# Kernel tuning notes

Hardware: AMD Instinct MI355X
Metric: run time of the kernel (lower is better)

Reference implementation:

```python
import jax, jax.numpy as jnp
import numpy as np

NH = 8  # num_heads
EPS_LN = 1e-5
BN_DENOM = float(np.sqrt(1.0 + 1e-5))  # eval-mode BN with running_mean=0, running_var=1


def _layernorm(x, g, b):
    m = jnp.mean(x, axis=-1, keepdims=True)
    v = jnp.var(x, axis=-1, keepdims=True)
    return (x - m) * jax.lax.rsqrt(v + EPS_LN) * g + b


def _rope(q, k):
    # q,k: [B, H, T, D]
    t, d = q.shape[2], q.shape[3]
    half = d // 2
    pos = jnp.arange(t, dtype=q.dtype)[:, None]
    idx = jnp.arange(half, dtype=q.dtype)[None, :]
    inv_freq = 1.0 / (10000.0 ** (idx / half))
    ang = pos * inv_freq  # [T, half]
    sin = jnp.sin(ang)[None, None]
    cos = jnp.cos(ang)[None, None]

    def rot(x):
        x1, x2 = x[..., :half], x[..., half:]
        return jnp.concatenate([x1 * cos - x2 * sin, x1 * sin + x2 * cos], axis=-1)

    return rot(q), rot(k)


def _sep_conv(y, dw, pw):
    # y: [B, C, T]; dw: [C, 1, K]; pw: [O, C]
    c = y.shape[1]
    k = dw.shape[-1]
    y = jax.lax.conv_general_dilated(
        y, dw, window_strides=(2,), padding=[(k // 2, k // 2)],
        dimension_numbers=('NCH', 'OIH', 'NCH'), feature_group_count=c)
    return jnp.einsum('bct,oc->bot', y, pw)


def _attn(h, Wq, bq, Wk, bk, Wv, bv, Wo, bo):
    b, t, e = h.shape
    hd = e // NH
    scale = hd ** -0.5

    def split(z):
        return jnp.transpose(z.reshape(b, t, NH, hd), (0, 2, 1, 3))

    q = split(h @ Wq.T + bq)
    k = split(h @ Wk.T + bk)
    v = split(h @ Wv.T + bv)
    q, k = _rope(q, k)
    logits = jnp.einsum('bhtd,bhsd->bhts', q, k) * scale
    attn = jax.nn.softmax(logits, axis=-1)
    ctx = jnp.einsum('bhts,bhsd->bhtd', attn, v)
    ctx = jnp.transpose(ctx, (0, 2, 1, 3)).reshape(b, t, e)
    return ctx @ Wo.T + bo


def setup_inputs() -> dict:
    key = jax.random.key(0)
    ks = jax.random.split(key, 40)
    B, T, Cin = 8, 4096, 64
    E, L, MLP = 256, 6, 1024
    s = 0.02
    p = {}
    p['x'] = jax.random.normal(ks[0], (B, T, Cin), jnp.float32)
    p['conv1_dw'] = jax.random.normal(ks[1], (Cin, 1, 7), jnp.float32) * s
    p['conv1_pw'] = jax.random.normal(ks[2], (64, Cin), jnp.float32) * s
    p['bn1_g'] = jnp.ones((64,), jnp.float32)
    p['bn1_b'] = jnp.zeros((64,), jnp.float32)
    p['conv2_dw'] = jax.random.normal(ks[3], (64, 1, 7), jnp.float32) * s
    p['conv2_pw'] = jax.random.normal(ks[4], (128, 64), jnp.float32) * s
    p['bn2_g'] = jnp.ones((128,), jnp.float32)
    p['bn2_b'] = jnp.zeros((128,), jnp.float32)
    p['proj_w'] = jax.random.normal(ks[5], (E, 128), jnp.float32) * s
    p['proj_b'] = jnp.zeros((E,), jnp.float32)
    p['cls_tok'] = jax.random.normal(ks[6], (1, 1, E), jnp.float32) * s
    p['Wq'] = jax.random.normal(ks[7], (L, E, E), jnp.float32) * s
    p['bq'] = jnp.zeros((L, E), jnp.float32)
    p['Wk'] = jax.random.normal(ks[8], (L, E, E), jnp.float32) * s
    p['bk'] = jnp.zeros((L, E), jnp.float32)
    p['Wv'] = jax.random.normal(ks[9], (L, E, E), jnp.float32) * s
    p['bv'] = jnp.zeros((L, E), jnp.float32)
    p['Wo'] = jax.random.normal(ks[10], (L, E, E), jnp.float32) * s
    p['bo'] = jnp.zeros((L, E), jnp.float32)
    p['ln1_g'] = jnp.ones((L, E), jnp.float32)
    p['ln1_b'] = jnp.zeros((L, E), jnp.float32)
    p['mlp_w1'] = jax.random.normal(ks[11], (L, MLP, E), jnp.float32) * s
    p['mlp_b1'] = jnp.zeros((L, MLP), jnp.float32)
    p['mlp_w2'] = jax.random.normal(ks[12], (L, E, MLP), jnp.float32) * s
    p['mlp_b2'] = jnp.zeros((L, E), jnp.float32)
    p['ln2_g'] = jnp.ones((L, E), jnp.float32)
    p['ln2_b'] = jnp.zeros((L, E), jnp.float32)
    p['lat_w'] = jax.random.normal(ks[13], (E, E), jnp.float32) * s
    p['lat_b'] = jnp.zeros((E,), jnp.float32)
    p['latn_g'] = jnp.ones((E,), jnp.float32)
    p['latn_b'] = jnp.zeros((E,), jnp.float32)
    p['ts_w'] = jax.random.normal(ks[14], (1, E), jnp.float32) * s
    p['ts_b'] = jnp.zeros((1,), jnp.float32)
    return p


def reference(x, conv1_dw, conv1_pw, bn1_g, bn1_b, conv2_dw, conv2_pw, bn2_g, bn2_b,
              proj_w, proj_b, cls_tok, Wq, bq, Wk, bk, Wv, bv, Wo, bo,
              ln1_g, ln1_b, mlp_w1, mlp_b1, mlp_w2, mlp_b2, ln2_g, ln2_b,
              lat_w, lat_b, latn_g, latn_b, ts_w, ts_b):
    B = x.shape[0]
    y = jnp.transpose(x, (0, 2, 1))  # [B, C, T]
    y = _sep_conv(y, conv1_dw, conv1_pw)
    y = (y / BN_DENOM) * bn1_g[None, :, None] + bn1_b[None, :, None]
    y = jax.nn.gelu(y, approximate=False)
    y = _sep_conv(y, conv2_dw, conv2_pw)
    y = (y / BN_DENOM) * bn2_g[None, :, None] + bn2_b[None, :, None]
    y = jax.nn.gelu(y, approximate=False)
    y = jnp.transpose(y, (0, 2, 1))  # [B, T', 128]
    h = y @ proj_w.T + proj_b  # [B, T', E]
    h = jnp.concatenate([jnp.broadcast_to(cls_tok, (B, 1, h.shape[-1])), h], axis=1)
    L = Wq.shape[0]
    for i in range(L):
        a = _attn(h, Wq[i], bq[i], Wk[i], bk[i], Wv[i], bv[i], Wo[i], bo[i])
        h = _layernorm(h + a, ln1_g[i], ln1_b[i])
        m = jax.nn.gelu(h @ mlp_w1[i].T + mlp_b1[i], approximate=False) @ mlp_w2[i].T + mlp_b2[i]
        h = _layernorm(h + m, ln2_g[i], ln2_b[i])
    h = _layernorm(h @ lat_w.T + lat_b, latn_g, latn_b)
    logits = h[:, 1:] @ ts_w.T + ts_b  # per-time-step logits (CLS excluded)
    return logits
```

## Files before the change

### kernel.cpp

```cpp
#include <hip/hip_runtime.h>
#include <hip/hip_bf16.h>
#include <math.h>

typedef __hip_bfloat16 bf16;
typedef __attribute__((ext_vector_type(8))) short bf16x8_t;
typedef __attribute__((ext_vector_type(4))) short bf16x4_t;
typedef __attribute__((ext_vector_type(4))) float f32x4_t;

#define BN_RDENOM 0.9999950000374997f
#define EPS_LN 1e-5f
#define ATTN_SCALE 0.17677669529663687f
#define S_LEN 1025
#define S_PAD 1088
#define E_DIM 256
#define NHEAD 8
#define HDIM 32
#define MROWS (8 * S_LEN)
#define M_PAD 8320
#define WSLOT 786432

__device__ __forceinline__ float bf(const bf16 v) { return __bfloat162float(v); }
__device__ __forceinline__ bf16 tobf(float v) { return __float2bfloat16(v); }
__device__ __forceinline__ short bfbits(float v) {
    bf16 t = __float2bfloat16(v); short s; __builtin_memcpy(&s, &t, 2); return s;
}
__device__ __forceinline__ float gelu_exact(float x) {
    return 0.5f * x * (1.0f + erff(x * 0.70710678118654752f));
}

#define DPP_ROR(x, N) __int_as_float(__builtin_amdgcn_update_dpp(0, __float_as_int(x), 0x120 + (N), 0xF, 0xF, false))
__device__ __forceinline__ float row_allsum(float x) {
    x = x + DPP_ROR(x, 1);
    x = x + DPP_ROR(x, 2);
    x = x + DPP_ROR(x, 4);
    x = x + DPP_ROR(x, 8);
    return x;
}

__global__ __launch_bounds__(256) void cvt_w(const float* __restrict__ src,
    bf16* __restrict__ dst, int n)
{
    int i = (blockIdx.x * 256 + threadIdx.x) * 4;
    if (i >= n) return;
    f32x4_t v = *(const f32x4_t*)(src + i);
    bf16x4_t o;
    #pragma unroll
    for (int j = 0; j < 4; ++j) o[j] = bfbits(v[j]);
    *(bf16x4_t*)((short*)dst + i) = o;
}

__global__ __launch_bounds__(256) void cvt_layer6(const float* __restrict__ wq,
    const float* __restrict__ wk, const float* __restrict__ wv, const float* __restrict__ wo,
    const float* __restrict__ w1, const float* __restrict__ w2, bf16* __restrict__ dst)
{
    int l = blockIdx.y;
    int i = (blockIdx.x * 256 + threadIdx.x) * 4;
    const float* s; int off;
    if (i < 262144) {
        s = (i < 65536) ? wq : (i < 131072) ? wk : (i < 196608) ? wv : wo;
        s += (size_t)l * 65536;
        off = i & 65535;
    } else if (i < 524288) { s = w1 + (size_t)l * 262144; off = i - 262144; }
    else                   { s = w2 + (size_t)l * 262144; off = i - 524288; }
    f32x4_t v = *(const f32x4_t*)(s + off);
    bf16x4_t o;
    #pragma unroll
    for (int j = 0; j < 4; ++j) o[j] = bfbits(v[j]);
    *(bf16x4_t*)((short*)dst + (size_t)l * WSLOT + i) = o;
}

__global__ __launch_bounds__(256) void conv_sep1(const float* __restrict__ x,
    const float* __restrict__ dw, const float* __restrict__ pw,
    const float* __restrict__ g, const float* __restrict__ bb,
    bf16* __restrict__ out)
{
    __shared__ float xs[70][64];
    __shared__ float dy[32][64];
    __shared__ float pws[64][65];
    __shared__ float dws[64][7];
    int blk = blockIdx.x;
    int tile = blk & 63, b = blk >> 6;
    int t0 = tile * 32;
    int tid = threadIdx.x;
    int tbase = t0 * 2 - 3;
    for (int i = tid; i < 70 * 64; i += 256) {
        int r = i >> 6, c = i & 63;
        int t = tbase + r;
        xs[r][c] = (t >= 0 && t < 4096) ? x[((size_t)b * 4096 + t) * 64 + c] : 0.f;
    }
    for (int i = tid; i < 64 * 7; i += 256) dws[i / 7][i % 7] = dw[i];
    for (int i = tid; i < 64 * 64; i += 256) pws[i >> 6][i & 63] = pw[i];
    __syncthreads();
    for (int i = tid; i < 32 * 64; i += 256) {
        int tl = i >> 6, c = i & 63;
        float s = 0.f;
        #pragma unroll
        for (int j = 0; j < 7; ++j) s += xs[2 * tl + j][c] * dws[c][j];
        dy[tl][c] = s;
    }
    __syncthreads();
    for (int i = tid; i < 32 * 64; i += 256) {
        int tl = i >> 6, o = i & 63;
        float s = 0.f;
        #pragma unroll 8
        for (int c = 0; c < 64; ++c) s += dy[tl][c] * pws[o][c];
        s = s * BN_RDENOM * g[o] + bb[o];
        out[((size_t)(b * 2048 + t0 + tl)) * 64 + o] = tobf(gelu_exact(s));
    }
}

__global__ __launch_bounds__(256) void conv_sep2(const bf16* __restrict__ x,
    const float* __restrict__ dw, const float* __restrict__ pw,
    const float* __restrict__ g, const float* __restrict__ bb,
    bf16* __restrict__ out)
{
    __shared__ float xs[70][64];
    __shared__ float dy[32][64];
    __shared__ float pws[128][65];
    __shared__ float dws[64][7];
    int blk = blockIdx.x;
    int tile = blk & 31, b = blk >> 5;
    int t0 = tile * 32;
    int tid = threadIdx.x;
    int tbase = t0 * 2 - 3;
    for (int i = tid; i < 70 * 64; i += 256) {
        int r = i >> 6, c = i & 63;
        int t = tbase + r;
        xs[r][c] = (t >= 0 && t < 2048) ? bf(x[((size_t)b * 2048 + t) * 64 + c]) : 0.f;
    }
    for (int i = tid; i < 64 * 7; i += 256) dws[i / 7][i % 7] = dw[i];
    for (int i = tid; i < 128 * 64; i += 256) pws[i >> 6][i & 63] = pw[i];
    __syncthreads();
    for (int i = tid; i < 32 * 64; i += 256) {
        int tl = i >> 6, c = i & 63;
        float s = 0.f;
        #pragma unroll
        for (int j = 0; j < 7; ++j) s += xs[2 * tl + j][c] * dws[c][j];
        dy[tl][c] = s;
    }
    __syncthreads();
    for (int i = tid; i < 32 * 128; i += 256) {
        int tl = i >> 7, o = i & 127;
        float s = 0.f;
        #pragma unroll 8
        for (int c = 0; c < 64; ++c) s += dy[tl][c] * pws[o][c];
        s = s * BN_RDENOM * g[o] + bb[o];
        out[((size_t)(b * 1024 + t0 + tl)) * 128 + o] = tobf(gelu_exact(s));
    }
}

template <int ACT>
__global__ __launch_bounds__(256) void gemm_bf(const bf16* __restrict__ A,
    const bf16* __restrict__ W, const float* __restrict__ bias,
    bf16* __restrict__ C, int M, int N, int K)
{
    __shared__ short As[64 * 72];
    __shared__ short Bs[64 * 72];
    int tid = threadIdx.x;
    int wave = tid >> 6, lane = tid & 63, quad = lane >> 4, l16 = lane & 15;
    int wm = wave & 1, wn = wave >> 1;
    int m0 = blockIdx.x * 64, n0 = blockIdx.y * 64;

    f32x4_t zero4 = {0.f, 0.f, 0.f, 0.f};
    f32x4_t acc[2][2];
    acc[0][0] = zero4; acc[0][1] = zero4; acc[1][0] = zero4; acc[1][1] = zero4;

    int srow = tid >> 2, skc = (tid & 3) * 16;
    for (int k0 = 0; k0 < K; k0 += 64) {
        {
            int m = m0 + srow;
            bf16x8_t a0 = {}, a1 = {};
            if (m < M) {
                a0 = *(const bf16x8_t*)(A + (size_t)m * K + k0 + skc);
                a1 = *(const bf16x8_t*)(A + (size_t)m * K + k0 + skc + 8);
            }
            *(bf16x8_t*)(&As[srow * 72 + skc])     = a0;
            *(bf16x8_t*)(&As[srow * 72 + skc + 8]) = a1;
        }
        {
            const bf16* wp = W + (size_t)(n0 + srow) * K + k0 + skc;
            *(bf16x8_t*)(&Bs[srow * 72 + skc])     = *(const bf16x8_t*)(wp);
            *(bf16x8_t*)(&Bs[srow * 72 + skc + 8]) = *(const bf16x8_t*)(wp + 8);
        }
        __syncthreads();
        #pragma unroll
        for (int ks = 0; ks < 2; ++ks) {
            bf16x8_t a[2], b[2];
            #pragma unroll
            for (int mi = 0; mi < 2; ++mi)
                a[mi] = *(bf16x8_t*)(&As[(wm * 32 + mi * 16 + l16) * 72 + ks * 32 + quad * 8]);
            #pragma unroll
            for (int ni = 0; ni < 2; ++ni)
                b[ni] = *(bf16x8_t*)(&Bs[(wn * 32 + ni * 16 + l16) * 72 + ks * 32 + quad * 8]);
            #pragma unroll
            for (int mi = 0; mi < 2; ++mi)
                #pragma unroll
                for (int ni = 0; ni < 2; ++ni)
                    acc[mi][ni] = __builtin_amdgcn_mfma_f32_16x16x32_bf16(a[mi], b[ni], acc[mi][ni], 0, 0, 0);
        }
        __syncthreads();
    }
    #pragma unroll
    for (int mi = 0; mi < 2; ++mi) {
        #pragma unroll
        for (int ni = 0; ni < 2; ++ni) {
            int col = n0 + wn * 32 + ni * 16 + l16;
            float bv = bias[col];
            #pragma unroll
            for (int r = 0; r < 4; ++r) {
                int row = m0 + wm * 32 + mi * 16 + quad * 4 + r;
                if (row < M) {
                    float v = acc[mi][ni][r] + bv;
                    if (ACT == 1) v = gelu_exact(v);
                    C[(size_t)row * N + col] = tobf(v);
                }
            }
        }
    }
}

template <int ACT>
__global__ __launch_bounds__(256) void gemm_bf128(const bf16* __restrict__ A,
    const bf16* __restrict__ W, const float* __restrict__ bias,
    bf16* __restrict__ C, int M, int N, int K)
{
    __shared__ short As[128 * 72];
    __shared__ short Bs[64 * 72];
    int tid = threadIdx.x;
    int wave = tid >> 6, lane = tid & 63, quad = lane >> 4, l16 = lane & 15;
    int wm = wave & 1, wn = wave >> 1;
    int m0 = blockIdx.x * 128, n0 = blockIdx.y * 64;

    f32x4_t zero4 = {0.f, 0.f, 0.f, 0.f};
    f32x4_t acc[4][2];
    #pragma unroll
    for (int i = 0; i < 4; ++i) { acc[i][0] = zero4; acc[i][1] = zero4; }

    int srow = tid >> 2, skc = (tid & 3) * 16;
    for (int k0 = 0; k0 < K; k0 += 64) {
        #pragma unroll
        for (int p = 0; p < 2; ++p) {
            int row = srow + p * 64;
            int m = m0 + row;
            bf16x8_t a0 = {}, a1 = {};
            if (m < M) {
                a0 = *(const bf16x8_t*)(A + (size_t)m * K + k0 + skc);
                a1 = *(const bf16x8_t*)(A + (size_t)m * K + k0 + skc + 8);
            }
            *(bf16x8_t*)(&As[row * 72 + skc])     = a0;
            *(bf16x8_t*)(&As[row * 72 + skc + 8]) = a1;
        }
        {
            const bf16* wp = W + (size_t)(n0 + srow) * K + k0 + skc;
            *(bf16x8_t*)(&Bs[srow * 72 + skc])     = *(const bf16x8_t*)(wp);
            *(bf16x8_t*)(&Bs[srow * 72 + skc + 8]) = *(const bf16x8_t*)(wp + 8);
        }
        __syncthreads();
        #pragma unroll
        for (int ks = 0; ks < 2; ++ks) {
            bf16x8_t a[4], b[2];
            #pragma unroll
            for (int mi = 0; mi < 4; ++mi)
                a[mi] = *(bf16x8_t*)(&As[(wm * 64 + mi * 16 + l16) * 72 + ks * 32 + quad * 8]);
            #pragma unroll
            for (int ni = 0; ni < 2; ++ni)
                b[ni] = *(bf16x8_t*)(&Bs[(wn * 32 + ni * 16 + l16) * 72 + ks * 32 + quad * 8]);
            #pragma unroll
            for (int mi = 0; mi < 4; ++mi)
                #pragma unroll
                for (int ni = 0; ni < 2; ++ni)
                    acc[mi][ni] = __builtin_amdgcn_mfma_f32_16x16x32_bf16(a[mi], b[ni], acc[mi][ni], 0, 0, 0);
        }
        __syncthreads();
    }
    #pragma unroll
    for (int mi = 0; mi < 4; ++mi) {
        #pragma unroll
        for (int ni = 0; ni < 2; ++ni) {
            int col = n0 + wn * 32 + ni * 16 + l16;
            float bv = bias[col];
            #pragma unroll
            for (int r = 0; r < 4; ++r) {
                int row = m0 + wm * 64 + mi * 16 + quad * 4 + r;
                if (row < M) {
                    float v = acc[mi][ni][r] + bv;
                    if (ACT == 1) v = gelu_exact(v);
                    C[(size_t)row * N + col] = tobf(v);
                }
            }
        }
    }
}

__global__ __launch_bounds__(256) void gemm_qkv128(const bf16* __restrict__ A,
    const bf16* __restrict__ Wqkv, const float* __restrict__ bq,
    const float* __restrict__ bk, const float* __restrict__ bv,
    bf16* __restrict__ qo, bf16* __restrict__ ko, bf16* __restrict__ vo, int M)
{
    const int K = 256, N = 256;
    __shared__ short As[128 * 72];
    __shared__ short Bs[64 * 72];
    int part = blockIdx.y >> 2;
    int n0 = (blockIdx.y & 3) * 64;
    const bf16* W     = Wqkv + (size_t)part * 65536;
    const float* bias = (part == 0) ? bq : (part == 1) ? bk : bv;
    float oscale = (part == 0) ? ATTN_SCALE : 1.0f;

    int tid = threadIdx.x;
    int wave = tid >> 6, lane = tid & 63, quad = lane >> 4, l16 = lane & 15;
    int wm = wave & 1, wn = wave >> 1;
    int m0 = blockIdx.x * 128;

    f32x4_t zero4 = {0.f, 0.f, 0.f, 0.f};
    f32x4_t acc[4][2];
    #pragma unroll
    for (int i = 0; i < 4; ++i) { acc[i][0] = zero4; acc[i][1] = zero4; }

    int srow = tid >> 2, skc = (tid & 3) * 16;
    for (int k0 = 0; k0 < K; k0 += 64) {
        #pragma unroll
        for (int p = 0; p < 2; ++p) {
            int row = srow + p * 64;
            int m = m0 + row;
            bf16x8_t a0 = {}, a1 = {};
            if (m < M) {
                a0 = *(const bf16x8_t*)(A + (size_t)m * K + k0 + skc);
                a1 = *(const bf16x8_t*)(A + (size_t)m * K + k0 + skc + 8);
            }
            *(bf16x8_t*)(&As[row * 72 + skc])     = a0;
            *(bf16x8_t*)(&As[row * 72 + skc + 8]) = a1;
        }
        {
            const bf16* wp = W + (size_t)(n0 + srow) * K + k0 + skc;
            *(bf16x8_t*)(&Bs[srow * 72 + skc])     = *(const bf16x8_t*)(wp);
            *(bf16x8_t*)(&Bs[srow * 72 + skc + 8]) = *(const bf16x8_t*)(wp + 8);
        }
        __syncthreads();
        #pragma unroll
        for (int ks = 0; ks < 2; ++ks) {
            bf16x8_t a[4], b[2];
            #pragma unroll
            for (int mi = 0; mi < 4; ++mi)
                a[mi] = *(bf16x8_t*)(&As[(wm * 64 + mi * 16 + l16) * 72 + ks * 32 + quad * 8]);
            #pragma unroll
            for (int ni = 0; ni < 2; ++ni)
                b[ni] = *(bf16x8_t*)(&Bs[(wn * 32 + ni * 16 + l16) * 72 + ks * 32 + quad * 8]);
            #pragma unroll
            for (int mi = 0; mi < 4; ++mi)
                #pragma unroll
                for (int ni = 0; ni < 2; ++ni)
                    acc[mi][ni] = __builtin_amdgcn_mfma_f32_16x16x32_bf16(a[mi], b[ni], acc[mi][ni], 0, 0, 0);
        }
        __syncthreads();
    }
    int col0 = n0 + wn * 32 + l16;
    float b1v = bias[col0], b2v = bias[col0 + 16];
    if (part == 2) {
        short* T = As;
        int colA = wn * 32 + l16;
        #pragma unroll
        for (int mi = 0; mi < 4; ++mi) {
            #pragma unroll
            for (int r = 0; r < 4; ++r) {
                int mrow = wm * 64 + mi * 16 + quad * 4 + r;
                T[colA * 136 + mrow]        = bfbits(acc[mi][0][r] + b1v);
                T[(colA + 16) * 136 + mrow] = bfbits(acc[mi][1][r] + b2v);
            }
        }
        __syncthreads();
        int c8 = tid >> 3, mo = (tid & 7) * 8;
        #pragma unroll
        for (int cc = 0; cc < 2; ++cc) {
            int col = c8 + cc * 32;
            int rowidx = ((n0 >> 5) + (col >> 5)) * HDIM + (col & 31);
            #pragma unroll
            for (int mm = 0; mm < 2; ++mm) {
                int m = mo + mm * 64;
                *(bf16x8_t*)(vo + (size_t)rowidx * M_PAD + m0 + m) =
                    *(bf16x8_t*)(&T[col * 136 + m]);
            }
        }
    } else {
        bf16* C = (part == 0) ? qo : ko;
        float invf = powf(10000.f, -(float)l16 * (1.f / 16.f));
        #pragma unroll
        for (int mi = 0; mi < 4; ++mi) {
            #pragma unroll
            for (int r = 0; r < 4; ++r) {
                int row = m0 + wm * 64 + mi * 16 + quad * 4 + r;
                if (row >= M) continue;
                int bb = row / S_LEN, t = row - bb * S_LEN;
                float x1 = acc[mi][0][r] + b1v;
                float x2 = acc[mi][1][r] + b2v;
                float ang = (float)t * invf;
                float sn, cs;
                __sincosf(ang, &sn, &cs);
                float y1 = (x1 * cs - x2 * sn) * oscale;
                float y2 = (x1 * sn + x2 * cs) * oscale;
                size_t obase = ((size_t)bb * S_PAD + t) * N;
                C[obase + col0]      = tobf(y1);
                C[obase + col0 + 16] = tobf(y2);
            }
        }
    }
}

__global__ __launch_bounds__(256) void assemble_h(const bf16* __restrict__ tmp,
    const float* __restrict__ cls, bf16* __restrict__ h)
{
    int row = blockIdx.x;
    int tid = threadIdx.x;
    int b = row / S_LEN, t = row % S_LEN;
    bf16 v = (t == 0) ? tobf(cls[tid]) : tmp[((size_t)(b * 1024 + t - 1)) * E_DIM + tid];
    h[(size_t)row * E_DIM + tid] = v;
}

__global__ __launch_bounds__(256) void attn_mfma(const bf16* __restrict__ Q,
    const bf16* __restrict__ K, const bf16* __restrict__ VT, bf16* __restrict__ O)
{
    __shared__ short Ks[2][64 * 40];
    __shared__ short Vs[2][32 * 72];
    __shared__ short Ps[4][16 * 72];
    int blk = blockIdx.x;
    int bh = blk & 63;
    int qt = blk >> 6;
    int hh = bh & 7, b = bh >> 3;
    int tid = threadIdx.x;
    int wave = tid >> 6, lane = tid & 63, quad = lane >> 4, l16 = lane & 15;
    int q0 = qt * 64 + wave * 16;
    const size_t bSp = (size_t)b * S_PAD;
    const size_t bS  = (size_t)b * S_LEN;
    const size_t hoff = (size_t)hh * HDIM;
    const bf16* Qb = Q + bSp * E_DIM + hoff;
    const bf16* Kb = K + bSp * E_DIM + hoff;

    f32x4_t zero4 = {0.f, 0.f, 0.f, 0.f};
    bf16x8_t qfrag = *(const bf16x8_t*)(Qb + (size_t)(q0 + l16) * E_DIM + quad * 8);
    f32x4_t o0 = zero4, o1 = zero4;
    float lsum[4] = {0.f, 0.f, 0.f, 0.f};
    short* myP = Ps[wave];

    int ksr = tid >> 2, kdc = (tid & 3) * 8;
    int vd  = tid >> 3, vsc = (tid & 7) * 8;
    const bf16* ksrc = Kb + (size_t)ksr * E_DIM + kdc;
    const bf16* vsrc = VT + ((size_t)(hh * HDIM + vd)) * M_PAD + bS + vsc;
    bf16x8_t kpre = *(const bf16x8_t*)(ksrc);
    bf16x8_t vpre = *(const bf16x8_t*)(vsrc);

    for (int c = 0; c < 17; ++c) {
        int s0 = c * 64;
        short* Kl = Ks[c & 1];
        short* Vl = Vs[c & 1];
        *(bf16x8_t*)(&Kl[ksr * 40 + kdc]) = kpre;
        *(bf16x8_t*)(&Vl[vd * 72 + vsc]) = vpre;
        __syncthreads();
        if (c < 16) {
            kpre = *(const bf16x8_t*)(ksrc + (size_t)(s0 + 64) * E_DIM);
            vpre = *(const bf16x8_t*)(vsrc + s0 + 64);
        }
        f32x4_t sc[4];
        #pragma unroll
        for (int kk = 0; kk < 4; ++kk) {
            bf16x8_t kf = *(bf16x8_t*)(&Kl[(kk * 16 + l16) * 40 + quad * 8]);
            sc[kk] = __builtin_amdgcn_mfma_f32_16x16x32_bf16(qfrag, kf, zero4, 0, 0, 0);
        }
        #pragma unroll
        for (int r = 0; r < 4; ++r) {
            float ps = 0.f;
            #pragma unroll
            for (int kk = 0; kk < 4; ++kk) {
                int s = s0 + kk * 16 + l16;
                float raw = (s < S_LEN) ? sc[kk][r] : -1e30f;
                float p = __expf(raw);
                ps += p;
                myP[(quad * 4 + r) * 72 + kk * 16 + l16] = bfbits(p);
            }
            lsum[r] += ps;
        }
        asm volatile("s_waitcnt lgkmcnt(0)" ::: "memory");
        __builtin_amdgcn_sched_barrier(0);
        #pragma unroll
        for (int half = 0; half < 2; ++half) {
            int off = half * 32 + quad * 8;
            bf16x8_t pf  = *(bf16x8_t*)(&myP[l16 * 72 + off]);
            bf16x8_t vf0 = *(bf16x8_t*)(&Vl[l16 * 72 + off]);
            bf16x8_t vf1 = *(bf16x8_t*)(&Vl[(16 + l16) * 72 + off]);
            o0 = __builtin_amdgcn_mfma_f32_16x16x32_bf16(pf, vf0, o0, 0, 0, 0);
            o1 = __builtin_amdgcn_mfma_f32_16x16x32_bf16(pf, vf1, o1, 0, 0, 0);
        }
    }
    #pragma unroll
    for (int r = 0; r < 4; ++r) {
        int qrow = q0 + quad * 4 + r;
        if (qrow < S_LEN) {
            float rs = 1.f / row_allsum(lsum[r]);
            O[(bS + qrow) * E_DIM + hoff + l16]      = tobf(o0[r] * rs);
            O[(bS + qrow) * E_DIM + hoff + 16 + l16] = tobf(o1[r] * rs);
        }
    }
}

__global__ __launch_bounds__(256) void ln_kernel(const bf16* __restrict__ X,
    const bf16* __restrict__ R, const float* __restrict__ g,
    const float* __restrict__ b, bf16* __restrict__ out)
{
    int wave = threadIdx.x >> 6, lane = threadIdx.x & 63;
    int row0 = blockIdx.x * 8 + wave * 2;
    size_t base0 = (size_t)row0 * E_DIM + lane * 4;
    size_t base1 = base0 + E_DIM;
    float v0[4], v1[4];
    {
        bf16x4_t xa = *(const bf16x4_t*)(X + base0);
        bf16x4_t xb = *(const bf16x4_t*)(X + base1);
        #pragma unroll
        for (int i = 0; i < 4; ++i) {
            bf16 t; short s;
            s = xa[i]; __builtin_memcpy(&t, &s, 2); v0[i] = bf(t);
            s = xb[i]; __builtin_memcpy(&t, &s, 2); v1[i] = bf(t);
        }
    }
    if (R) {
        bf16x4_t ra = *(const bf16x4_t*)(R + base0);
        bf16x4_t rb = *(const bf16x4_t*)(R + base1);
        #pragma unroll
        for (int i = 0; i < 4; ++i) {
            bf16 t; short s;
            s = ra[i]; __builtin_memcpy(&t, &s, 2); v0[i] += bf(t);
            s = rb[i]; __builtin_memcpy(&t, &s, 2); v1[i] += bf(t);
        }
    }
    float s0 = v0[0] + v0[1] + v0[2] + v0[3];
    float s1 = v1[0] + v1[1] + v1[2] + v1[3];
    #pragma unroll
    for (int off = 32; off; off >>= 1) { s0 += __shfl_xor(s0, off); s1 += __shfl_xor(s1, off); }
    float m0 = s0 * (1.f / 256.f), m1 = s1 * (1.f / 256.f);
    float w0 = 0.f, w1 = 0.f;
    #pragma unroll
    for (int i = 0; i < 4; ++i) {
        v0[i] -= m0; w0 += v0[i] * v0[i];
        v1[i] -= m1; w1 += v1[i] * v1[i];
    }
    #pragma unroll
    for (int off = 32; off; off >>= 1) { w0 += __shfl_xor(w0, off); w1 += __shfl_xor(w1, off); }
    float r0 = rsqrtf(w0 * (1.f / 256.f) + EPS_LN);
    float r1 = rsqrtf(w1 * (1.f / 256.f) + EPS_LN);
    int c = lane * 4;
    bf16x4_t oa, ob;
    #pragma unroll
    for (int i = 0; i < 4; ++i) {
        oa[i] = bfbits(v0[i] * r0 * g[c + i] + b[c + i]);
        ob[i] = bfbits(v1[i] * r1 * g[c + i] + b[c + i]);
    }
    *(bf16x4_t*)(out + base0) = oa;
    *(bf16x4_t*)(out + base1) = ob;
}

__global__ __launch_bounds__(256) void ts_kernel(const bf16* __restrict__ H,
    const float* __restrict__ w, const float* __restrict__ tb,
    float* __restrict__ out)
{
    int wid = (blockIdx.x << 2) + (threadIdx.x >> 6);
    int lane = threadIdx.x & 63;
    int b = wid >> 10, t = wid & 1023;
    const bf16* row = H + ((size_t)(b * S_LEN + t + 1)) * E_DIM;
    float acc = 0.f;
    for (int e = lane; e < E_DIM; e += 64) acc += bf(row[e]) * w[e];
    #pragma unroll
    for (int off = 32; off; off >>= 1) acc += __shfl_down(acc, off, 64);
    if (lane == 0) out[wid] = acc + tb[0];
}

extern "C" void kernel_launch(void* const* d_in, const int* in_sizes, int n_in,
                              void* d_out, int out_size, void* d_ws, size_t ws_size,
                              hipStream_t stream)
{
    (void)in_sizes; (void)n_in; (void)out_size; (void)ws_size;
    const float* X        = (const float*)d_in[0];
    const float* CONV1_DW = (const float*)d_in[1];
    const float* CONV1_PW = (const float*)d_in[2];
    const float* BN1_G    = (const float*)d_in[3];
    const float* BN1_B    = (const float*)d_in[4];
    const float* CONV2_DW = (const float*)d_in[5];
    const float* CONV2_PW = (const float*)d_in[6];
    const float* BN2_G    = (const float*)d_in[7];
    const float* BN2_B    = (const float*)d_in[8];
    const float* PROJ_W   = (const float*)d_in[9];
    const float* PROJ_B   = (const float*)d_in[10];
    const float* CLS      = (const float*)d_in[11];
    const float* WQ       = (const float*)d_in[12];
    const float* BQ       = (const float*)d_in[13];
    const float* WK       = (const float*)d_in[14];
    const float* BK       = (const float*)d_in[15];
    const float* WV       = (const float*)d_in[16];
    const float* BV       = (const float*)d_in[17];
    const float* WO       = (const float*)d_in[18];
    const float* BO       = (const float*)d_in[19];
    const float* LN1G     = (const float*)d_in[20];
    const float* LN1B     = (const float*)d_in[21];
    const float* W1       = (const float*)d_in[22];
    const float* B1       = (const float*)d_in[23];
    const float* W2       = (const float*)d_in[24];
    const float* B2       = (const float*)d_in[25];
    const float* LN2G     = (const float*)d_in[26];
    const float* LN2B     = (const float*)d_in[27];
    const float* LATW     = (const float*)d_in[28];
    const float* LATB     = (const float*)d_in[29];
    const float* LATNG    = (const float*)d_in[30];
    const float* LATNB    = (const float*)d_in[31];
    const float* TSW      = (const float*)d_in[32];
    const float* TSB      = (const float*)d_in[33];

    const size_t SROW  = (size_t)MROWS * E_DIM;
    const size_t SPROW = (size_t)8 * S_PAD * E_DIM;
    bf16* h    = (bf16*)d_ws;
    bf16* bufB = h + SROW;
    bf16* r0   = bufB + SROW;
    bf16* q  = r0;
    bf16* k  = r0 + SPROW;
    bf16* v  = r0 + 2 * SPROW;
    bf16* cx = r0 + 3 * SPROW;
    bf16* wall = cx + SROW;
    bf16* pslot = wall + 6 * WSLOT;
    bf16* y1 = r0;
    bf16* y2 = r0 + SROW;
    bf16* mid = r0;

    conv_sep1<<<dim3(512), dim3(256), 0, stream>>>(X, CONV1_DW, CONV1_PW, BN1_G, BN1_B, y1);
    conv_sep2<<<dim3(256), dim3(256), 0, stream>>>(y1, CONV2_DW, CONV2_PW, BN2_G, BN2_B, y2);
    cvt_w<<<dim3(32), dim3(256), 0, stream>>>(PROJ_W, pslot, 32768);
    gemm_bf<0><<<dim3(128, 4), dim3(256), 0, stream>>>(y2, pslot, PROJ_B, bufB, 8192, 256, 128);
    assemble_h<<<dim3(MROWS), dim3(256), 0, stream>>>(bufB, CLS, h);
    cvt_layer6<<<dim3(768, 6), dim3(256), 0, stream>>>(WQ, WK, WV, WO, W1, W2, wall);

    for (int l = 0; l < 6; ++l) {
        bf16* wslot = wall + (size_t)l * WSLOT;
        gemm_qkv128<<<dim3(65, 12), dim3(256), 0, stream>>>(h, wslot,
            BQ + l * 256, BK + l * 256, BV + l * 256, q, k, v, MROWS);
        attn_mfma<<<dim3(64 * 17), dim3(256), 0, stream>>>(q, k, v, cx);
        gemm_bf<0><<<dim3(129, 4), dim3(256), 0, stream>>>(cx, wslot + 196608, BO + l * 256, bufB, MROWS, 256, 256);
        ln_kernel<<<dim3(MROWS / 8), dim3(256), 0, stream>>>(h, bufB, LN1G + l * 256, LN1B + l * 256, h);
        gemm_bf128<1><<<dim3(65, 16), dim3(256), 0, stream>>>(h, wslot + 262144, B1 + l * 1024, mid, MROWS, 1024, 256);
        gemm_bf<0><<<dim3(129, 4), dim3(256), 0, stream>>>(mid, wslot + 524288, B2 + l * 256, bufB, MROWS, 256, 1024);
        ln_kernel<<<dim3(MROWS / 8), dim3(256), 0, stream>>>(h, bufB, LN2G + l * 256, LN2B + l * 256, h);
    }

    cvt_w<<<dim3(64), dim3(256), 0, stream>>>(LATW, pslot, 65536);
    gemm_bf<0><<<dim3(129, 4), dim3(256), 0, stream>>>(h, pslot, LATB, bufB, MROWS, 256, 256);
    ln_kernel<<<dim3(MROWS / 8), dim3(256), 0, stream>>>(bufB, nullptr, LATNG, LATNB, r0);
    ts_kernel<<<dim3(2048), dim3(256), 0, stream>>>(r0, TSW, TSB, (float*)d_out);
}
```

Measured before the change: 762.8 us.

## Process two 16-row query groups per wave in attention to reuse K/V tiles

Each wave in the attention kernel now handles 32 query rows instead of 16, so each block covers 128 queries and the grid shrinks from 1088 to 576 blocks. K fragments are loaded from LDS once and used for both query groups, and V fragments are shared across the two PV MFMAs. This halves the global and LDS traffic for K/V per query. In exchange it adds register pressure, doubles the P scratch in LDS, and leaves fewer blocks to fill the GPU.

```diff
diff --git a/kernel.cpp b/kernel.cpp
--- a/kernel.cpp
+++ b/kernel.cpp
@@ -420,14 +420,14 @@
 {
     __shared__ short Ks[2][64 * 40];
     __shared__ short Vs[2][32 * 72];
-    __shared__ short Ps[4][16 * 72];
+    __shared__ short Ps[4][32 * 72];
     int blk = blockIdx.x;
     int bh = blk & 63;
     int qt = blk >> 6;
     int hh = bh & 7, b = bh >> 3;
     int tid = threadIdx.x;
     int wave = tid >> 6, lane = tid & 63, quad = lane >> 4, l16 = lane & 15;
-    int q0 = qt * 64 + wave * 16;
+    int q0 = qt * 128 + wave * 32;
     const size_t bSp = (size_t)b * S_PAD;
     const size_t bS  = (size_t)b * S_LEN;
     const size_t hoff = (size_t)hh * HDIM;
@@ -435,9 +435,16 @@
     const bf16* Kb = K + bSp * E_DIM + hoff;
 
     f32x4_t zero4 = {0.f, 0.f, 0.f, 0.f};
-    bf16x8_t qfrag = *(const bf16x8_t*)(Qb + (size_t)(q0 + l16) * E_DIM + quad * 8);
-    f32x4_t o0 = zero4, o1 = zero4;
-    float lsum[4] = {0.f, 0.f, 0.f, 0.f};
+    bf16x8_t qfrag[2];
+    #pragma unroll
+    for (int g = 0; g < 2; ++g) {
+        int qr = q0 + g * 16 + l16;
+        if (qr >= S_LEN) qr = 0;
+        qfrag[g] = *(const bf16x8_t*)(Qb + (size_t)qr * E_DIM + quad * 8);
+    }
+    f32x4_t o0[2], o1[2];
+    o0[0] = zero4; o0[1] = zero4; o1[0] = zero4; o1[1] = zero4;
+    float lsum[2][4] = {{0.f, 0.f, 0.f, 0.f}, {0.f, 0.f, 0.f, 0.f}};
     short* myP = Ps[wave];
 
     int ksr = tid >> 2, kdc = (tid & 3) * 8;
@@ -458,44 +465,55 @@
             kpre = *(const bf16x8_t*)(ksrc + (size_t)(s0 + 64) * E_DIM);
             vpre = *(const bf16x8_t*)(vsrc + s0 + 64);
         }
-        f32x4_t sc[4];
-        #pragma unroll
-        for (int kk = 0; kk < 4; ++kk) {
-            bf16x8_t kf = *(bf16x8_t*)(&Kl[(kk * 16 + l16) * 40 + quad * 8]);
-            sc[kk] = __builtin_amdgcn_mfma_f32_16x16x32_bf16(qfrag, kf, zero4, 0, 0, 0);
-        }
-        #pragma unroll
-        for (int r = 0; r < 4; ++r) {
-            float ps = 0.f;
-            #pragma unroll
-            for (int kk = 0; kk < 4; ++kk) {
-                int s = s0 + kk * 16 + l16;
-                float raw = (s < S_LEN) ? sc[kk][r] : -1e30f;
-                float p = __expf(raw);
-                ps += p;
-                myP[(quad * 4 + r) * 72 + kk * 16 + l16] = bfbits(p);
-            }
-            lsum[r] += ps;
+        bf16x8_t kf[4];
+        #pragma unroll
+        for (int kk = 0; kk < 4; ++kk)
+            kf[kk] = *(bf16x8_t*)(&Kl[(kk * 16 + l16) * 40 + quad * 8]);
+        #pragma unroll
+        for (int g = 0; g < 2; ++g) {
+            f32x4_t sc[4];
+            #pragma unroll
+            for (int kk = 0; kk < 4; ++kk)
+                sc[kk] = __builtin_amdgcn_mfma_f32_16x16x32_bf16(qfrag[g], kf[kk], zero4, 0, 0, 0);
+            #pragma unroll
+            for (int r = 0; r < 4; ++r) {
+                float ps = 0.f;
+                #pragma unroll
+                for (int kk = 0; kk < 4; ++kk) {
+                    int s = s0 + kk * 16 + l16;
+                    float raw = (s < S_LEN) ? sc[kk][r] : -1e30f;
+                    float p = __expf(raw);
+                    ps += p;
+                    myP[(g * 16 + quad * 4 + r) * 72 + kk * 16 + l16] = bfbits(p);
+                }
+                lsum[g][r] += ps;
+            }
         }
         asm volatile("s_waitcnt lgkmcnt(0)" ::: "memory");
         __builtin_amdgcn_sched_barrier(0);
         #pragma unroll
         for (int half = 0; half < 2; ++half) {
             int off = half * 32 + quad * 8;
-            bf16x8_t pf  = *(bf16x8_t*)(&myP[l16 * 72 + off]);
             bf16x8_t vf0 = *(bf16x8_t*)(&Vl[l16 * 72 + off]);
             bf16x8_t vf1 = *(bf16x8_t*)(&Vl[(16 + l16) * 72 + off]);
-            o0 = __builtin_amdgcn_mfma_f32_16x16x32_bf16(pf, vf0, o0, 0, 0, 0);
-            o1 = __builtin_amdgcn_mfma_f32_16x16x32_bf16(pf, vf1, o1, 0, 0, 0);
-        }
-    }
-    #pragma unroll
-    for (int r = 0; r < 4; ++r) {
-        int qrow = q0 + quad * 4 + r;
-        if (qrow < S_LEN) {
-            float rs = 1.f / row_allsum(lsum[r]);
-            O[(bS + qrow) * E_DIM + hoff + l16]      = tobf(o0[r] * rs);
-            O[(bS + qrow) * E_DIM + hoff + 16 + l16] = tobf(o1[r] * rs);
+            #pragma unroll
+            for (int g = 0; g < 2; ++g) {
+                bf16x8_t pf = *(bf16x8_t*)(&myP[(g * 16 + l16) * 72 + off]);
+                o0[g] = __builtin_amdgcn_mfma_f32_16x16x32_bf16(pf, vf0, o0[g], 0, 0, 0);
+                o1[g] = __builtin_amdgcn_mfma_f32_16x16x32_bf16(pf, vf1, o1[g], 0, 0, 0);
+            }
+        }
+    }
+    #pragma unroll
+    for (int g = 0; g < 2; ++g) {
+        #pragma unroll
+        for (int r = 0; r < 4; ++r) {
+            int qrow = q0 + g * 16 + quad * 4 + r;
+            if (qrow < S_LEN) {
+                float rs = 1.f / row_allsum(lsum[g][r]);
+                O[(bS + qrow) * E_DIM + hoff + l16]      = tobf(o0[g][r] * rs);
+                O[(bS + qrow) * E_DIM + hoff + 16 + l16] = tobf(o1[g][r] * rs);
+            }
         }
     }
 }
@@ -636,7 +654,7 @@
         bf16* wslot = wall + (size_t)l * WSLOT;
         gemm_qkv128<<<dim3(65, 12), dim3(256), 0, stream>>>(h, wslot,
             BQ + l * 256, BK + l * 256, BV + l * 256, q, k, v, MROWS);
-        attn_mfma<<<dim3(64 * 17), dim3(256), 0, stream>>>(q, k, v, cx);
+        attn_mfma<<<dim3(64 * 9), dim3(256), 0, stream>>>(q, k, v, cx);
         gemm_bf<0><<<dim3(129, 4), dim3(256), 0, stream>>>(cx, wslot + 196608, BO + l * 256, bufB, MROWS, 256, 256);
         ln_kernel<<<dim3(MROWS / 8), dim3(256), 0, stream>>>(h, bufB, LN1G + l * 256, LN1B + l * 256, h);
         gemm_bf128<1><<<dim3(65, 16), dim3(256), 0, stream>>>(h, wslot + 262144, B1 + l * 1024, mid, MROWS, 1024, 256);
```

After: 774.2 us. No clear change (+1.5%).

## Fuse residual add and LayerNorm into full-row output GEMM epilogue

Applied to the files above, without the earlier changes.

Adds a GEMM kernel where each block computes a full 32x256 output row tile, then adds bias and the residual and applies LayerNorm in the epilogue through a cross-wave reduction in shared memory. It replaces the Wo, MLP-down and latent GEMMs together with their separate LayerNorm kernels, which removes a bf16 intermediate write and read and one launch per fusion. In exchange the grid shrinks to 257 blocks, each reloading the full 256-row weight tile, and the variance is computed as E[x^2]-mean^2, which is less numerically robust. The kernel reads the residual from h and writes the output back into h in place.

```diff
diff --git a/kernel.cpp b/kernel.cpp
--- a/kernel.cpp
+++ b/kernel.cpp
@@ -287,6 +287,113 @@
                     if (ACT == 1) v = gelu_exact(v);
                     C[(size_t)row * N + col] = tobf(v);
                 }
+            }
+        }
+    }
+}
+
+template <int RES>
+__global__ __launch_bounds__(256) void gemm_resln(const bf16* __restrict__ A,
+    const bf16* __restrict__ W, const float* __restrict__ bias,
+    const bf16* __restrict__ R, const float* __restrict__ g,
+    const float* __restrict__ bb, bf16* __restrict__ out, int M, int K)
+{
+    const int N = 256;
+    __shared__ short As[32 * 72];
+    __shared__ short Bs[256 * 72];
+    __shared__ float red[2][32][4];
+    int tid = threadIdx.x;
+    int wn = tid >> 6, lane = tid & 63, quad = lane >> 4, l16 = lane & 15;
+    int m0 = blockIdx.x * 32;
+
+    f32x4_t zero4 = {0.f, 0.f, 0.f, 0.f};
+    f32x4_t acc[2][4];
+    #pragma unroll
+    for (int mi = 0; mi < 2; ++mi)
+        #pragma unroll
+        for (int ni = 0; ni < 4; ++ni) acc[mi][ni] = zero4;
+
+    int ar = tid >> 3, akc = (tid & 7) * 8;
+    int am = m0 + ar; if (am >= M) am = M - 1;
+    const bf16* asrc = A + (size_t)am * K + akc;
+    const bf16* bsrc = W + (size_t)ar * K + akc;
+
+    bf16x8_t apre = *(const bf16x8_t*)(asrc);
+    bf16x8_t bpre[8];
+    #pragma unroll
+    for (int p = 0; p < 8; ++p)
+        bpre[p] = *(const bf16x8_t*)(bsrc + (size_t)(p * 32) * K);
+
+    for (int k0 = 0; k0 < K; k0 += 64) {
+        *(bf16x8_t*)(&As[ar * 72 + akc]) = apre;
+        #pragma unroll
+        for (int p = 0; p < 8; ++p)
+            *(bf16x8_t*)(&Bs[(p * 32 + ar) * 72 + akc]) = bpre[p];
+        __syncthreads();
+        if (k0 + 64 < K) {
+            apre = *(const bf16x8_t*)(asrc + k0 + 64);
+            #pragma unroll
+            for (int p = 0; p < 8; ++p)
+                bpre[p] = *(const bf16x8_t*)(bsrc + (size_t)(p * 32) * K + k0 + 64);
+        }
+        #pragma unroll
+        for (int ks = 0; ks < 2; ++ks) {
+            bf16x8_t a[2], b[4];
+            #pragma unroll
+            for (int mi = 0; mi < 2; ++mi)
+                a[mi] = *(bf16x8_t*)(&As[(mi * 16 + l16) * 72 + ks * 32 + quad * 8]);
+            #pragma unroll
+            for (int ni = 0; ni < 4; ++ni)
+                b[ni] = *(bf16x8_t*)(&Bs[(wn * 64 + ni * 16 + l16) * 72 + ks * 32 + quad * 8]);
+            #pragma unroll
+            for (int mi = 0; mi < 2; ++mi)
+                #pragma unroll
+                for (int ni = 0; ni < 4; ++ni)
+                    acc[mi][ni] = __builtin_amdgcn_mfma_f32_16x16x32_bf16(a[mi], b[ni], acc[mi][ni], 0, 0, 0);
+        }
+        __syncthreads();
+    }
+    float v[2][4][4];
+    float bcol[4];
+    #pragma unroll
+    for (int ni = 0; ni < 4; ++ni) bcol[ni] = bias[wn * 64 + ni * 16 + l16];
+    #pragma unroll
+    for (int mi = 0; mi < 2; ++mi) {
+        #pragma unroll
+        for (int r = 0; r < 4; ++r) {
+            int row = mi * 16 + quad * 4 + r;
+            int mrow = m0 + row;
+            float s = 0.f, s2 = 0.f;
+            #pragma unroll
+            for (int ni = 0; ni < 4; ++ni) {
+                float x = acc[mi][ni][r] + bcol[ni];
+                if (RES && mrow < M)
+                    x += bf(R[(size_t)mrow * N + wn * 64 + ni * 16 + l16]);
+                v[mi][ni][r] = x;
+                s += x; s2 += x * x;
+            }
+            s = row_allsum(s); s2 = row_allsum(s2);
+            if (l16 == 0) { red[0][row][wn] = s; red[1][row][wn] = s2; }
+        }
+    }
+    __syncthreads();
+    #pragma unroll
+    for (int mi = 0; mi < 2; ++mi) {
+        #pragma unroll
+        for (int r = 0; r < 4; ++r) {
+            int row = mi * 16 + quad * 4 + r;
+            int mrow = m0 + row;
+            if (mrow >= M) continue;
+            float sum = red[0][row][0] + red[0][row][1] + red[0][row][2] + red[0][row][3];
+            float sq  = red[1][row][0] + red[1][row][1] + red[1][row][2] + red[1][row][3];
+            float mean = sum * (1.f / 256.f);
+            float var  = sq * (1.f / 256.f) - mean * mean;
+            float rstd = rsqrtf(var + EPS_LN);
+            #pragma unroll
+            for (int ni = 0; ni < 4; ++ni) {
+                int col = wn * 64 + ni * 16 + l16;
+                out[(size_t)mrow * N + col] =
+                    tobf((v[mi][ni][r] - mean) * rstd * g[col] + bb[col]);
             }
         }
     }
@@ -498,61 +605,6 @@
             O[(bS + qrow) * E_DIM + hoff + 16 + l16] = tobf(o1[r] * rs);
         }
     }
-}
-
-__global__ __launch_bounds__(256) void ln_kernel(const bf16* __restrict__ X,
-    const bf16* __restrict__ R, const float* __restrict__ g,
-    const float* __restrict__ b, bf16* __restrict__ out)
-{
-    int wave = threadIdx.x >> 6, lane = threadIdx.x & 63;
-    int row0 = blockIdx.x * 8 + wave * 2;
-    size_t base0 = (size_t)row0 * E_DIM + lane * 4;
-    size_t base1 = base0 + E_DIM;
-    float v0[4], v1[4];
-    {
-        bf16x4_t xa = *(const bf16x4_t*)(X + base0);
-        bf16x4_t xb = *(const bf16x4_t*)(X + base1);
-        #pragma unroll
-        for (int i = 0; i < 4; ++i) {
-            bf16 t; short s;
-            s = xa[i]; __builtin_memcpy(&t, &s, 2); v0[i] = bf(t);
-            s = xb[i]; __builtin_memcpy(&t, &s, 2); v1[i] = bf(t);
-        }
-    }
-    if (R) {
-        bf16x4_t ra = *(const bf16x4_t*)(R + base0);
-        bf16x4_t rb = *(const bf16x4_t*)(R + base1);
-        #pragma unroll
-        for (int i = 0; i < 4; ++i) {
-            bf16 t; short s;
-            s = ra[i]; __builtin_memcpy(&t, &s, 2); v0[i] += bf(t);
-            s = rb[i]; __builtin_memcpy(&t, &s, 2); v1[i] += bf(t);
-        }
-    }
-    float s0 = v0[0] + v0[1] + v0[2] + v0[3];
-    float s1 = v1[0] + v1[1] + v1[2] + v1[3];
-    #pragma unroll
-    for (int off = 32; off; off >>= 1) { s0 += __shfl_xor(s0, off); s1 += __shfl_xor(s1, off); }
-    float m0 = s0 * (1.f / 256.f), m1 = s1 * (1.f / 256.f);
-    float w0 = 0.f, w1 = 0.f;
-    #pragma unroll
-    for (int i = 0; i < 4; ++i) {
-        v0[i] -= m0; w0 += v0[i] * v0[i];
-        v1[i] -= m1; w1 += v1[i] * v1[i];
-    }
-    #pragma unroll
-    for (int off = 32; off; off >>= 1) { w0 += __shfl_xor(w0, off); w1 += __shfl_xor(w1, off); }
-    float r0 = rsqrtf(w0 * (1.f / 256.f) + EPS_LN);
-    float r1 = rsqrtf(w1 * (1.f / 256.f) + EPS_LN);
-    int c = lane * 4;
-    bf16x4_t oa, ob;
-    #pragma unroll
-    for (int i = 0; i < 4; ++i) {
-        oa[i] = bfbits(v0[i] * r0 * g[c + i] + b[c + i]);
-        ob[i] = bfbits(v1[i] * r1 * g[c + i] + b[c + i]);
-    }
-    *(bf16x4_t*)(out + base0) = oa;
-    *(bf16x4_t*)(out + base1) = ob;
 }
 
 __global__ __launch_bounds__(256) void ts_kernel(const bf16* __restrict__ H,
@@ -637,15 +689,15 @@
         gemm_qkv128<<<dim3(65, 12), dim3(256), 0, stream>>>(h, wslot,
             BQ + l * 256, BK + l * 256, BV + l * 256, q, k, v, MROWS);
         attn_mfma<<<dim3(64 * 17), dim3(256), 0, stream>>>(q, k, v, cx);
-        gemm_bf<0><<<dim3(129, 4), dim3(256), 0, stream>>>(cx, wslot + 196608, BO + l * 256, bufB, MROWS, 256, 256);
-        ln_kernel<<<dim3(MROWS / 8), dim3(256), 0, stream>>>(h, bufB, LN1G + l * 256, LN1B + l * 256, h);
+        gemm_resln<1><<<dim3(257), dim3(256), 0, stream>>>(cx, wslot + 196608,
+            BO + l * 256, h, LN1G + l * 256, LN1B + l * 256, h, MROWS, 256);
         gemm_bf128<1><<<dim3(65, 16), dim3(256), 0, stream>>>(h, wslot + 262144, B1 + l * 1024, mid, MROWS, 1024, 256);
-        gemm_bf<0><<<dim3(129, 4), dim3(256), 0, stream>>>(mid, wslot + 524288, B2 + l * 256, bufB, MROWS, 256, 1024);
-        ln_kernel<<<dim3(MROWS / 8), dim3(256), 0, stream>>>(h, bufB, LN2G + l * 256, LN2B + l * 256, h);
+        gemm_resln<1><<<dim3(257), dim3(256), 0, stream>>>(mid, wslot + 524288,
+            B2 + l * 256, h, LN2G + l * 256, LN2B + l * 256, h, MROWS, 1024);
     }
 
     cvt_w<<<dim3(64), dim3(256), 0, stream>>>(LATW, pslot, 65536);
-    gemm_bf<0><<<dim3(129, 4), dim3(256), 0, stream>>>(h, pslot, LATB, bufB, MROWS, 256, 256);
-    ln_kernel<<<dim3(MROWS / 8), dim3(256), 0, stream>>>(bufB, nullptr, LATNG, LATNB, r0);
+    gemm_resln<0><<<dim3(257), dim3(256), 0, stream>>>(h, pslot, LATB, nullptr,
+        LATNG, LATNB, r0, MROWS, 256);
     ts_kernel<<<dim3(2048), dim3(256), 0, stream>>>(r0, TSW, TSB, (float*)d_out);
 }
```

Result: no change. 765.0 us (+0.3%).
